# Kernel tuning notes

Hardware: AMD Instinct MI355X
Metric: run time of the kernel (lower is better)

## Reference

```python
import jax, jax.numpy as jnp
import numpy as np

EMBED_DIM = 1024
NUM_HEADS = 16
HEAD_DIM = EMBED_DIM // NUM_HEADS
LN_EPS = 1e-5


def setup_inputs() -> dict:
    key = jax.random.key(0)
    ks = jax.random.split(key, 12)
    B, SQ, SKV, E = 2, 1024, 4096, EMBED_DIM
    s = 1.0 / np.sqrt(E)
    return {
        "query": jax.random.normal(ks[0], (B, SQ, E), jnp.float32),
        "key_value": jax.random.normal(ks[1], (B, SKV, E), jnp.float32),
        "key_value_mask": jax.random.randint(ks[2], (B, SKV), 0, 2, jnp.int32),
        "Wq": jax.random.normal(ks[3], (E, E), jnp.float32) * s,
        "bq": jnp.zeros((E,), jnp.float32),
        "Wk": jax.random.normal(ks[4], (E, E), jnp.float32) * s,
        "bk": jnp.zeros((E,), jnp.float32),
        "Wv": jax.random.normal(ks[5], (E, E), jnp.float32) * s,
        "bv": jnp.zeros((E,), jnp.float32),
        "Wo": jax.random.normal(ks[6], (E, E), jnp.float32) * s,
        "bo": jnp.zeros((E,), jnp.float32),
        "ln_gamma": jnp.ones((E,), jnp.float32),
        "ln_beta": jnp.zeros((E,), jnp.float32),
    }


def reference(query, key_value, key_value_mask, Wq, bq, Wk, bk, Wv, bv, Wo, bo, ln_gamma, ln_beta):
    B, SQ, E = query.shape
    SKV = key_value.shape[1]
    H, D = NUM_HEADS, HEAD_DIM
    # projections (dropout is eval-mode identity)
    q = (query @ Wq.T + bq).reshape(B, SQ, H, D).transpose(0, 2, 1, 3)      # b h sq d
    k = (key_value @ Wk.T + bk).reshape(B, SKV, H, D).transpose(0, 2, 1, 3)  # b h skv d
    v = (key_value @ Wv.T + bv).reshape(B, SKV, H, D).transpose(0, 2, 1, 3)
    scale = jnp.sqrt(jnp.asarray(D, q.dtype))
    scores = jnp.einsum('bhqd,bhkd->bhqk', q, k) / scale                     # b h sq skv
    mask = (key_value_mask != 0)[:, None, None, :]                           # b 1 1 skv
    scores = jnp.where(mask, scores, jnp.asarray(-jnp.inf, scores.dtype))
    attn = jax.nn.softmax(scores, axis=-1)
    out = jnp.einsum('bhqk,bhkd->bhqd', attn, v)
    out = out.transpose(0, 2, 1, 3).reshape(B, SQ, E)
    out = out @ Wo.T + bo
    # post-LN residual
    x = query + out
    mu = jnp.mean(x, axis=-1, keepdims=True)
    var = jnp.mean(jnp.square(x - mu), axis=-1, keepdims=True)
    return (x - mu) * jax.lax.rsqrt(var + LN_EPS) * ln_gamma + ln_beta
```

## Files before the change

### kernel.cpp

```cpp
#include <hip/hip_runtime.h>
#include <cstdint>


typedef __bf16 bf16x8_t  __attribute__((ext_vector_type(8)));
typedef float  f32x4_t   __attribute__((ext_vector_type(4)));
typedef float  f32x16_t  __attribute__((ext_vector_type(16)));

#define E_DIM 1024
#define NH    16
#define HD    64
#define SCALE_L2E 0.1803368804f

__device__ __forceinline__ unsigned short f32_bf16(float f) {
    union { float f; unsigned int u; } v; v.f = f;
    unsigned int u = v.u;
    unsigned int r = (u + 0x7fffu + ((u >> 16) & 1u)) >> 16;
    return (unsigned short)r;
}

__device__ __forceinline__ unsigned pack_bf16(float a, float b) {
    __bf16 x = (__bf16)a, y = (__bf16)b;
    unsigned short ux = __builtin_bit_cast(unsigned short, x);
    unsigned short uy = __builtin_bit_cast(unsigned short, y);
    return (unsigned)ux | ((unsigned)uy << 16);
}

__device__ __forceinline__ void gld16(const unsigned short* g, unsigned short* l) {
    __builtin_amdgcn_global_load_lds(
        (const __attribute__((address_space(1))) unsigned int*)g,
        (__attribute__((address_space(3))) unsigned int*)l, 16, 0, 0);
}

__device__ __forceinline__ bf16x8_t ld16g(const unsigned short* p) {
    union { uint4 u; bf16x8_t f; } v;
    v.u = *reinterpret_cast<const uint4*>(p);
    return v.f;
}

__global__ void cast_all(const float* __restrict__ q, const float* __restrict__ kv,
                         const float* __restrict__ wq, const float* __restrict__ wk,
                         const float* __restrict__ wv, const float* __restrict__ wo,
                         unsigned short* __restrict__ Xq, unsigned short* __restrict__ Xkv,
                         unsigned short* __restrict__ Wqb, unsigned short* __restrict__ Wkb,
                         unsigned short* __restrict__ Wvb, unsigned short* __restrict__ Wob,
                         const int* __restrict__ msk, float* __restrict__ Sub) {
    __shared__ int red[4];
    if (blockIdx.x >= 14336) {
        int b = blockIdx.x - 14336, t = threadIdx.x;
        int s = 0;
#pragma unroll
        for (int k = 0; k < 16; k++) s += (msk[b * 4096 + k * 256 + t] != 0);
#pragma unroll
        for (int off = 32; off >= 1; off >>= 1) s += __shfl_xor(s, off, 64);
        if ((t & 63) == 0) red[t >> 6] = s;
        __syncthreads();
        if (t == 0)
            Sub[b] = (float)(4096 - (red[0] + red[1] + red[2] + red[3]));
        return;
    }
    long i = (long)blockIdx.x * 256 + threadIdx.x;
    const float* src; unsigned short* dst; long off;
    if (i < 2621440) {
        if (i < 524288) { src = q;  dst = Xq;  off = i; }
        else            { src = kv; dst = Xkv; off = i - 524288; }
    } else {
        long j = i - 2621440;
        int w = (int)(j >> 18); off = j & 262143;
        src = (w == 0) ? wq : (w == 1) ? wk : (w == 2) ? wv : wo;
        dst = (w == 0) ? Wqb : (w == 1) ? Wkb : (w == 2) ? Wvb : Wob;
    }
    float4 v = reinterpret_cast<const float4*>(src)[off];
    ushort4 o;
    o.x = f32_bf16(v.x); o.y = f32_bf16(v.y);
    o.z = f32_bf16(v.z); o.w = f32_bf16(v.w);
    reinterpret_cast<ushort4*>(dst)[off] = o;
}

#define BK 64

__global__ __launch_bounds__(256) void gemm_qkv(
    const unsigned short* __restrict__ Xq,
    const unsigned short* __restrict__ Xkv,
    const unsigned short* __restrict__ Wqb,
    const unsigned short* __restrict__ Wkb,
    const unsigned short* __restrict__ Wvb,
    const float* __restrict__ bq,
    const float* __restrict__ bk,
    const float* __restrict__ bv,
    unsigned short* __restrict__ Qout,
    unsigned short* __restrict__ Kout,
    unsigned short* __restrict__ Vout,
    const int* __restrict__ kvm)
{
    __shared__ __align__(16) unsigned short As[128 * BK];
    __shared__ __align__(16) unsigned short Bs[128 * BK];
    int bid  = blockIdx.x;
    int tid  = threadIdx.x;
    int lane = tid & 63;
    int wvu  = __builtin_amdgcn_readfirstlane(tid >> 6);
    int l15  = lane & 15, quad = lane >> 4, x7 = l15 & 7;

    if (bid < 1024) {
        int xcd  = bid & 7;
        int j    = bid >> 3;
        int mt   = xcd * 8 + (j >> 4);
        int sel  = j & 15;
        int isV  = sel >= 8;
        int m0   = mt * 128;
        int n0   = (sel & 7) * 128;
        const unsigned short* W = isV ? Wvb : Wkb;
        const float* bias = isV ? bv : bk;
        int wm   = ((tid >> 6) >> 1) * 64, wn = ((tid >> 6) & 1) * 64;

        f32x4_t acc[4][4];
#pragma unroll
        for (int i = 0; i < 4; i++)
#pragma unroll
            for (int jj = 0; jj < 4; jj++) acc[i][jj] = (f32x4_t)(0.f);

        for (int k0 = 0; k0 < 1024; k0 += BK) {
            __syncthreads();
#pragma unroll
            for (int i = 0; i < 4; i++) {
                int s = (i * 4 + wvu) * 64 + lane;
                int row = s >> 3, pcol = ((s & 7) ^ (row & 7)) << 3;
                gld16(&Xkv[(long)(m0 + row) * 1024 + k0 + pcol], &As[(i * 4 + wvu) * 512]);
                gld16(&W[(long)(n0 + row) * 1024 + k0 + pcol], &Bs[(i * 4 + wvu) * 512]);
            }
            __syncthreads();
            const char* Ab = (const char*)As;
            const char* Bb = (const char*)Bs;
#pragma unroll
            for (int ks = 0; ks < 2; ks++) {
                int pos = (((ks << 2) + quad) ^ x7) << 4;
                bf16x8_t af[4], bf[4];
#pragma unroll
                for (int mi = 0; mi < 4; mi++)
                    af[mi] = *reinterpret_cast<const bf16x8_t*>(
                        Ab + (wm + mi * 16 + l15) * 128 + pos);
#pragma unroll
                for (int ni = 0; ni < 4; ni++)
                    bf[ni] = *reinterpret_cast<const bf16x8_t*>(
                        Bb + (wn + ni * 16 + l15) * 128 + pos);
#pragma unroll
                for (int mi = 0; mi < 4; mi++)
#pragma unroll
                    for (int ni = 0; ni < 4; ni++)
                        acc[mi][ni] = __builtin_amdgcn_mfma_f32_16x16x32_bf16(
                            af[mi], bf[ni], acc[mi][ni], 0, 0, 0);
            }
        }
        int4 mk[4];
#pragma unroll
        for (int mi = 0; mi < 4; mi++) {
            int mg0 = m0 + wm + mi * 16 + quad * 4;
            mk[mi] = *reinterpret_cast<const int4*>(&kvm[mg0]);
        }
        if (!isV) {
#pragma unroll
            for (int mi = 0; mi < 4; mi++)
#pragma unroll
                for (int ni = 0; ni < 4; ni++) {
                    int n = n0 + wn + ni * 16 + l15;
                    float bvv = bias[n];
                    int h = n >> 6, d = n & 63;
#pragma unroll
                    for (int r = 0; r < 4; r++) {
                        int mg = m0 + wm + mi * 16 + quad * 4 + r;
                        int b = mg >> 12, s = mg & 4095;
                        unsigned short val = (&mk[mi].x)[r]
                            ? f32_bf16(acc[mi][ni][r] + bvv) : (unsigned short)0;
                        Kout[(((b * NH + h) << 12) + s) * HD + d] = val;
                    }
                }
        } else {
#pragma unroll
            for (int mi = 0; mi < 4; mi++)
#pragma unroll
                for (int ni = 0; ni < 4; ni++) {
                    int n = n0 + wn + ni * 16 + l15;
                    float bvv = bias[n];
                    int h = n >> 6, d = n & 63;
                    int mg0 = m0 + wm + mi * 16 + quad * 4;
                    int b = mg0 >> 12, s = mg0 & 4095;
                    ushort4 w;
                    w.x = mk[mi].x ? f32_bf16(acc[mi][ni][0] + bvv) : (unsigned short)0;
                    w.y = mk[mi].y ? f32_bf16(acc[mi][ni][1] + bvv) : (unsigned short)0;
                    w.z = mk[mi].z ? f32_bf16(acc[mi][ni][2] + bvv) : (unsigned short)0;
                    w.w = mk[mi].w ? f32_bf16(acc[mi][ni][3] + bvv) : (unsigned short)0;
                    *reinterpret_cast<ushort4*>(
                        &Vout[(((b * NH + h) * HD + d) << 12) + s]) = w;
                }
        }
    } else {
        int t    = bid - 1024;
        int xcd  = bid & 7;
        int j    = t >> 3;
        int mt   = xcd * 4 + (j >> 3);
        int m0   = mt * 64;
        int n0   = (j & 7) * 128;
        int wm   = ((tid >> 6) >> 1) * 32, wn = ((tid >> 6) & 1) * 64;

        f32x4_t acc[2][4];
#pragma unroll
        for (int i = 0; i < 2; i++)
#pragma unroll
            for (int jj = 0; jj < 4; jj++) acc[i][jj] = (f32x4_t)(0.f);

        for (int k0 = 0; k0 < 1024; k0 += BK) {
            __syncthreads();
#pragma unroll
            for (int i = 0; i < 2; i++) {
                int s = (i * 4 + wvu) * 64 + lane;
                int row = s >> 3, pcol = ((s & 7) ^ (row & 7)) << 3;
                gld16(&Xq[(long)(m0 + row) * 1024 + k0 + pcol], &As[(i * 4 + wvu) * 512]);
            }
#pragma unroll
            for (int i = 0; i < 4; i++) {
                int s = (i * 4 + wvu) * 64 + lane;
                int row = s >> 3, pcol = ((s & 7) ^ (row & 7)) << 3;
                gld16(&Wqb[(long)(n0 + row) * 1024 + k0 + pcol], &Bs[(i * 4 + wvu) * 512]);
            }
            __syncthreads();
            const char* Ab = (const char*)As;
            const char* Bb = (const char*)Bs;
#pragma unroll
            for (int ks = 0; ks < 2; ks++) {
                int pos = (((ks << 2) + quad) ^ x7) << 4;
                bf16x8_t af[2], bf[4];
#pragma unroll
                for (int mi = 0; mi < 2; mi++)
                    af[mi] = *reinterpret_cast<const bf16x8_t*>(
                        Ab + (wm + mi * 16 + l15) * 128 + pos);
#pragma unroll
                for (int ni = 0; ni < 4; ni++)
                    bf[ni] = *reinterpret_cast<const bf16x8_t*>(
                        Bb + (wn + ni * 16 + l15) * 128 + pos);
#pragma unroll
                for (int mi = 0; mi < 2; mi++)
#pragma unroll
                    for (int ni = 0; ni < 4; ni++)
                        acc[mi][ni] = __builtin_amdgcn_mfma_f32_16x16x32_bf16(
                            af[mi], bf[ni], acc[mi][ni], 0, 0, 0);
            }
        }
#pragma unroll
        for (int mi = 0; mi < 2; mi++)
#pragma unroll
            for (int ni = 0; ni < 4; ni++) {
                int n = n0 + wn + ni * 16 + l15;
                float bvq = bq[n];
                int h = n >> 6, d = n & 63;
#pragma unroll
                for (int r = 0; r < 4; r++) {
                    int mg = m0 + wm + mi * 16 + quad * 4 + r;
                    int b = mg >> 10, s = mg & 1023;
                    Qout[(((b * NH + h) << 10) + s) * HD + d] =
                        f32_bf16((acc[mi][ni][r] + bvq) * SCALE_L2E);
                }
            }
    }
}

__global__ __launch_bounds__(256) void gemm_oproj(
    const unsigned short* __restrict__ A,
    const unsigned short* __restrict__ W,
    const float* __restrict__ bias,
    const float* __restrict__ resid,
    float* __restrict__ xout)
{
    __shared__ __align__(16) unsigned short As[32 * BK];
    __shared__ __align__(16) unsigned short Bs[64 * BK];
    int tid  = threadIdx.x;
    int m0   = blockIdx.y * 32;
    int n0   = blockIdx.x * 64;
    int lane = tid & 63;
    int wvu  = __builtin_amdgcn_readfirstlane(tid >> 6);
    int l15  = lane & 15, quad = lane >> 4, x7 = l15 & 7;
    int wn   = (tid >> 6) * 16;

    f32x4_t acc[2];
    acc[0] = (f32x4_t)(0.f); acc[1] = (f32x4_t)(0.f);

    for (int k0 = 0; k0 < 1024; k0 += BK) {
        __syncthreads();
        {
            int s = wvu * 64 + lane;
            int row = s >> 3, pcol = ((s & 7) ^ (row & 7)) << 3;
            gld16(&A[(long)(m0 + row) * 1024 + k0 + pcol], &As[wvu * 512]);
        }
#pragma unroll
        for (int i = 0; i < 2; i++) {
            int s = (i * 4 + wvu) * 64 + lane;
            int row = s >> 3, pcol = ((s & 7) ^ (row & 7)) << 3;
            gld16(&W[(long)(n0 + row) * 1024 + k0 + pcol], &Bs[(i * 4 + wvu) * 512]);
        }
        __syncthreads();
        const char* Ab = (const char*)As;
        const char* Bb = (const char*)Bs;
#pragma unroll
        for (int ks = 0; ks < 2; ks++) {
            int pos = (((ks << 2) + quad) ^ x7) << 4;
            bf16x8_t af[2], bf;
#pragma unroll
            for (int mi = 0; mi < 2; mi++)
                af[mi] = *reinterpret_cast<const bf16x8_t*>(
                    Ab + (mi * 16 + l15) * 128 + pos);
            bf = *reinterpret_cast<const bf16x8_t*>(
                Bb + (wn + l15) * 128 + pos);
#pragma unroll
            for (int mi = 0; mi < 2; mi++)
                acc[mi] = __builtin_amdgcn_mfma_f32_16x16x32_bf16(
                    af[mi], bf, acc[mi], 0, 0, 0);
        }
    }
    int n = n0 + wn + l15;
    float bv = bias[n];
#pragma unroll
    for (int mi = 0; mi < 2; mi++)
#pragma unroll
        for (int r = 0; r < 4; r++) {
            int mg = m0 + mi * 16 + quad * 4 + r;
            xout[mg * 1024 + n] = acc[mi][r] + bv + resid[mg * 1024 + n];
        }
}

__global__ __launch_bounds__(512, 4) void attn_kernel(
    const unsigned short* __restrict__ Q,
    const unsigned short* __restrict__ K,
    const unsigned short* __restrict__ VT,
    float* __restrict__ Osc,
    float* __restrict__ Lsc)
{
    __shared__ __align__(16) union {
        struct { unsigned short Kb[2][8192]; unsigned short Vb[2][8192]; } st;
        struct { float OL[4][2048]; float ls[128]; } mg;
    } sm;

    int tid  = threadIdx.x;
    int lane = tid & 63;
    int w    = tid >> 6;
    int wvu  = __builtin_amdgcn_readfirstlane(w);
    int l31  = lane & 31, hw = lane >> 5;
    int qsub = w & 3, kvsub = w >> 2;

    int bid  = blockIdx.x;
    int xcd  = bid & 7, gidx = bid >> 3;
    int bh   = xcd * 4 + (gidx & 3);
    int rest = gidx >> 2;
    int q0   = (rest & 7) * 128;
    int bhalf = rest >> 3;

    const unsigned short* Kg = K + ((long)bh * 4096 + bhalf * 2048) * HD;
    const unsigned short* Vg = VT + (long)bh * HD * 4096 + bhalf * 2048;
    const unsigned short* Qb = Q + ((long)bh * 1024 + q0) * HD;

    bf16x8_t qfr[4];
#pragma unroll
    for (int ks = 0; ks < 4; ks++)
        qfr[ks] = ld16g(Qb + (qsub * 32 + l31) * HD + ks * 16 + hw * 8);

    f32x16_t oacc[2];
    oacc[0] = (f32x16_t)(0.f); oacc[1] = (f32x16_t)(0.f);
    float l_run = 0.f;

    auto stage = [&](int kt, int bufi) {
#pragma unroll
        for (int i = 0; i < 2; i++) {
            int s = (i * 8 + wvu) * 64 + lane;
            int krow = s >> 3, kpc = ((s & 7) ^ (krow & 7)) << 3;
            gld16(&Kg[(long)(kt * 128 + krow) * HD + kpc],
                  &sm.st.Kb[bufi][(i * 8 + wvu) * 512]);
            int vrow = s >> 4, vpc = ((s & 15) ^ (vrow & 15)) << 3;
            gld16(&Vg[(long)vrow * 4096 + kt * 128 + vpc],
                  &sm.st.Vb[bufi][(i * 8 + wvu) * 512]);
        }
    };

    const char* Kc = (const char*)sm.st.Kb;
    const char* Vc = (const char*)sm.st.Vb;

    stage(0, 0);
#pragma unroll 2
    for (int kt = 0; kt < 16; kt++) {
        __syncthreads();
        if (kt + 1 < 16) stage(kt + 1, (kt + 1) & 1);
        int bo = (kt & 1) * 16384;

#pragma unroll
        for (int t = 0; t < 2; t++) {
            f32x16_t sa = (f32x16_t)(0.f);
            int krow = kvsub * 64 + t * 32 + l31;
            __builtin_amdgcn_s_setprio(1);
#pragma unroll
            for (int ks = 0; ks < 4; ks++) {
                int phys = (ks * 2 + hw) ^ (krow & 7);
                bf16x8_t kf = *reinterpret_cast<const bf16x8_t*>(
                    Kc + bo + krow * 128 + phys * 16);
                sa = __builtin_amdgcn_mfma_f32_32x32x16_bf16(kf, qfr[ks], sa, 0, 0, 0);
            }
            __builtin_amdgcn_s_setprio(0);

            float pv[16];
#pragma unroll
            for (int r = 0; r < 16; r++) {
                float e;
                asm("v_exp_f32 %0, %1" : "=v"(e) : "v"(sa[r]));
                pv[r] = e;
            }
            float s0 = (pv[0] + pv[1]) + (pv[2] + pv[3]);
            float s1 = (pv[4] + pv[5]) + (pv[6] + pv[7]);
            float s2 = (pv[8] + pv[9]) + (pv[10] + pv[11]);
            float s3 = (pv[12] + pv[13]) + (pv[14] + pv[15]);
            l_run += (s0 + s1) + (s2 + s3);
            unsigned pku[8];
#pragma unroll
            for (int s4 = 0; s4 < 4; s4++) {
                pku[s4 * 2 + 0] = pack_bf16(pv[s4 * 4 + 0], pv[s4 * 4 + 1]);
                pku[s4 * 2 + 1] = pack_bf16(pv[s4 * 4 + 2], pv[s4 * 4 + 3]);
            }

            __builtin_amdgcn_s_setprio(1);
#pragma unroll
            for (int ks2 = 0; ks2 < 2; ks2++) {
                unsigned x0 = pku[(ks2 * 2) * 2 + 0];
                unsigned x1 = pku[(ks2 * 2) * 2 + 1];
                unsigned z0 = pku[(ks2 * 2 + 1) * 2 + 0];
                unsigned z1 = pku[(ks2 * 2 + 1) * 2 + 1];
                asm("v_permlane32_swap_b32 %0, %1" : "+v"(x0), "+v"(z0));
                asm("v_permlane32_swap_b32 %0, %1" : "+v"(x1), "+v"(z1));
                union { uint4 u; bf16x8_t f; } bw;
                bw.u.x = x0; bw.u.y = x1; bw.u.z = z0; bw.u.w = z1;
                int c = kvsub * 8 + t * 4 + ks2 * 2 + hw;
#pragma unroll
                for (int ds = 0; ds < 2; ds++) {
                    int vrow = ds * 32 + l31;
                    int phys = c ^ (vrow & 15);
                    bf16x8_t va = *reinterpret_cast<const bf16x8_t*>(
                        Vc + bo + vrow * 256 + phys * 16);
                    oacc[ds] = __builtin_amdgcn_mfma_f32_32x32x16_bf16(
                        va, bw.f, oacc[ds], 0, 0, 0);
                }
            }
            __builtin_amdgcn_s_setprio(0);
        }
    }

    l_run += __shfl_xor(l_run, 32, 64);
    __syncthreads();
    if (kvsub == 1) {
        float* OL = sm.mg.OL[qsub];
#pragma unroll
        for (int ds = 0; ds < 2; ds++)
#pragma unroll
            for (int r = 0; r < 16; r++) {
                int d = ds * 32 + (r & 3) + 8 * (r >> 2) + 4 * hw;
                OL[d * 32 + l31] = oacc[ds][r];
            }
        if (hw == 0) sm.mg.ls[qsub * 32 + l31] = l_run;
    }
    __syncthreads();
    if (kvsub == 0) {
        const float* OL = sm.mg.OL[qsub];
        int q = q0 + qsub * 32 + l31;
        long obase = (((long)bhalf * 32 + bh) * 64) * 1024;
#pragma unroll
        for (int ds = 0; ds < 2; ds++)
#pragma unroll
            for (int r = 0; r < 16; r++) {
                int d = ds * 32 + (r & 3) + 8 * (r >> 2) + 4 * hw;
                Osc[obase + (long)d * 1024 + q] = oacc[ds][r] + OL[d * 32 + l31];
            }
        if (hw == 0)
            Lsc[((long)bhalf * 32 + bh) * 1024 + q] = l_run + sm.mg.ls[qsub * 32 + l31];
    }
}

__global__ __launch_bounds__(256) void attn_merge(
    const float* __restrict__ Osc, const float* __restrict__ Lsc,
    const float* __restrict__ Sub, unsigned short* __restrict__ AO)
{
    __shared__ unsigned short T[64 * 66];
    int t = threadIdx.x, w = t >> 6, lane = t & 63;
    int bh = blockIdx.y, b = bh >> 4, h = bh & 15;
    int q0 = blockIdx.x * 64;
    int q = q0 + lane;

    float ls = Lsc[(long)bh * 1024 + q]
             + Lsc[(long)(32 + bh) * 1024 + q] - Sub[b];
    float inv = __builtin_amdgcn_rcpf(ls);
    inv = inv * (2.f - ls * inv);

#pragma unroll
    for (int dd = 0; dd < 16; dd++) {
        int d = w * 16 + dd;
        long base = (long)bh * 64 * 1024 + (long)d * 1024 + q;
        float o = Osc[base] + Osc[base + 32l * 64 * 1024];
        T[lane * 66 + d] = f32_bf16(o * inv);
    }
    __syncthreads();
    int q2 = t >> 2, c16 = (t & 3) * 16;
    unsigned ov[8];
#pragma unroll
    for (int j = 0; j < 8; j++)
        ov[j] = *reinterpret_cast<const unsigned*>(&T[q2 * 66 + c16 + j * 2]);
    unsigned short* dst = &AO[((long)(b * 1024 + q0 + q2)) * E_DIM + h * HD + c16];
    reinterpret_cast<uint4*>(dst)[0] = make_uint4(ov[0], ov[1], ov[2], ov[3]);
    reinterpret_cast<uint4*>(dst)[1] = make_uint4(ov[4], ov[5], ov[6], ov[7]);
}

__global__ __launch_bounds__(256) void ln_kernel(
    const float* __restrict__ x, const float* __restrict__ g,
    const float* __restrict__ be, float* __restrict__ out)
{
    __shared__ float red[8];
    int row = blockIdx.x, tid = threadIdx.x;
    float4 v = reinterpret_cast<const float4*>(x)[row * 256 + tid];
    float s  = v.x + v.y + v.z + v.w;
    float sq = v.x * v.x + v.y * v.y + v.z * v.z + v.w * v.w;
#pragma unroll
    for (int off = 32; off >= 1; off >>= 1) {
        s  += __shfl_xor(s,  off, 64);
        sq += __shfl_xor(sq, off, 64);
    }
    if ((tid & 63) == 0) { red[tid >> 6] = s; red[4 + (tid >> 6)] = sq; }
    __syncthreads();
    s  = red[0] + red[1] + red[2] + red[3];
    sq = red[4] + red[5] + red[6] + red[7];
    float mu  = s * (1.f / 1024.f);
    float var = sq * (1.f / 1024.f) - mu * mu;
    float rs  = rsqrtf(var + 1e-5f);
    int c = tid * 4;
    float4 o;
    o.x = (v.x - mu) * rs * g[c]     + be[c];
    o.y = (v.y - mu) * rs * g[c + 1] + be[c + 1];
    o.z = (v.z - mu) * rs * g[c + 2] + be[c + 2];
    o.w = (v.w - mu) * rs * g[c + 3] + be[c + 3];
    reinterpret_cast<float4*>(out)[row * 256 + tid] = o;
}

extern "C" void kernel_launch(void* const* d_in, const int* in_sizes, int n_in,
                              void* d_out, int out_size, void* d_ws, size_t ws_size,
                              hipStream_t stream) {
    const float* query     = (const float*)d_in[0];
    const float* key_value = (const float*)d_in[1];
    const int*   kv_mask   = (const int*)d_in[2];
    const float* Wq = (const float*)d_in[3];
    const float* bq = (const float*)d_in[4];
    const float* Wk = (const float*)d_in[5];
    const float* bk = (const float*)d_in[6];
    const float* Wv = (const float*)d_in[7];
    const float* bv = (const float*)d_in[8];
    const float* Wo = (const float*)d_in[9];
    const float* bo = (const float*)d_in[10];
    const float* ln_g = (const float*)d_in[11];
    const float* ln_b = (const float*)d_in[12];
    float* out = (float*)d_out;

    char* ws = (char*)d_ws;
    unsigned short* Xq  = (unsigned short*)(ws);
    unsigned short* Xkv = (unsigned short*)(ws + (4ll  << 20));
    unsigned short* Wqb = (unsigned short*)(ws + (20ll << 20));
    unsigned short* Wkb = (unsigned short*)(ws + (22ll << 20));
    unsigned short* Wvb = (unsigned short*)(ws + (24ll << 20));
    float*          Osc = (float*)(ws);
    unsigned short* Kh  = (unsigned short*)(ws + (32ll << 20));
    unsigned short* VTh = (unsigned short*)(ws + (48ll << 20));
    unsigned short* AO  = (unsigned short*)(ws + (64ll << 20));
    float*          Xr  = (float*)(ws + (68ll << 20));
    float*          Lsc = (float*)(ws + (76ll << 20));
    float*          Sub = (float*)(ws + (77ll << 20));
    unsigned short* Qh  = (unsigned short*)(ws + (80ll << 20));
    unsigned short* Wob = (unsigned short*)(ws + (84ll << 20));

    cast_all<<<14338, 256, 0, stream>>>(query, key_value, Wq, Wk, Wv, Wo,
                                        Xq, Xkv, Wqb, Wkb, Wvb, Wob,
                                        kv_mask, Sub);

    gemm_qkv<<<1280, 256, 0, stream>>>(Xq, Xkv, Wqb, Wkb, Wvb, bq, bk, bv,
                                       Qh, Kh, VTh, kv_mask);

    attn_kernel<<<512, 512, 0, stream>>>(Qh, Kh, VTh, Osc, Lsc);
    attn_merge<<<dim3(16, 32), 256, 0, stream>>>(Osc, Lsc, Sub, AO);

    gemm_oproj<<<dim3(16, 64), 256, 0, stream>>>(AO, Wob, bo, query, Xr);

    ln_kernel<<<2048, 256, 0, stream>>>(Xr, ln_g, ln_b, out);
}
```

Measured before the change: 234.9 us.

## Fuse attention split-KV merge into attention kernel by splitting KV across waves

Each block now covers 64 queries over the full 4096-key range instead of 128 queries over half the keys. The KV split moves inside the block across four wave groups, which are reduced through shared memory. The normalized bf16 output is written to AO directly, so the fp32 partial-output and row-sum buffers and the separate merge kernel go away. The costs are a 4-way shared-memory reduction instead of a 2-way one, and each block now streams twice as many K/V tiles for half as many queries, which doubles total K/V traffic.

```diff
diff --git a/kernel.cpp b/kernel.cpp
--- a/kernel.cpp
+++ b/kernel.cpp
@@ -329,12 +329,12 @@
     const unsigned short* __restrict__ Q,
     const unsigned short* __restrict__ K,
     const unsigned short* __restrict__ VT,
-    float* __restrict__ Osc,
-    float* __restrict__ Lsc)
+    const float* __restrict__ Sub,
+    unsigned short* __restrict__ AO)
 {
     __shared__ __align__(16) union {
         struct { unsigned short Kb[2][8192]; unsigned short Vb[2][8192]; } st;
-        struct { float OL[4][2048]; float ls[128]; } mg;
+        struct { float OL[6][2048]; float ls[256]; unsigned short T[64 * 66]; } mg;
     } sm;
 
     int tid  = threadIdx.x;
@@ -342,17 +342,16 @@
     int w    = tid >> 6;
     int wvu  = __builtin_amdgcn_readfirstlane(w);
     int l31  = lane & 31, hw = lane >> 5;
-    int qsub = w & 3, kvsub = w >> 2;
+    int qsub = w & 1, kvsub = w >> 1;
 
     int bid  = blockIdx.x;
     int xcd  = bid & 7, gidx = bid >> 3;
     int bh   = xcd * 4 + (gidx & 3);
-    int rest = gidx >> 2;
-    int q0   = (rest & 7) * 128;
-    int bhalf = rest >> 3;
-
-    const unsigned short* Kg = K + ((long)bh * 4096 + bhalf * 2048) * HD;
-    const unsigned short* Vg = VT + (long)bh * HD * 4096 + bhalf * 2048;
+    int q0   = (gidx >> 2) * 64;
+    int b    = bh >> 4, h = bh & 15;
+
+    const unsigned short* Kg = K + (long)bh * 4096 * HD;
+    const unsigned short* Vg = VT + (long)bh * HD * 4096;
     const unsigned short* Qb = Q + ((long)bh * 1024 + q0) * HD;
 
     bf16x8_t qfr[4];
@@ -382,74 +381,71 @@
 
     stage(0, 0);
 #pragma unroll 2
-    for (int kt = 0; kt < 16; kt++) {
+    for (int kt = 0; kt < 32; kt++) {
         __syncthreads();
-        if (kt + 1 < 16) stage(kt + 1, (kt + 1) & 1);
+        if (kt + 1 < 32) stage(kt + 1, (kt + 1) & 1);
         int bo = (kt & 1) * 16384;
 
-#pragma unroll
-        for (int t = 0; t < 2; t++) {
-            f32x16_t sa = (f32x16_t)(0.f);
-            int krow = kvsub * 64 + t * 32 + l31;
-            __builtin_amdgcn_s_setprio(1);
-#pragma unroll
-            for (int ks = 0; ks < 4; ks++) {
-                int phys = (ks * 2 + hw) ^ (krow & 7);
-                bf16x8_t kf = *reinterpret_cast<const bf16x8_t*>(
-                    Kc + bo + krow * 128 + phys * 16);
-                sa = __builtin_amdgcn_mfma_f32_32x32x16_bf16(kf, qfr[ks], sa, 0, 0, 0);
-            }
-            __builtin_amdgcn_s_setprio(0);
-
-            float pv[16];
-#pragma unroll
-            for (int r = 0; r < 16; r++) {
-                float e;
-                asm("v_exp_f32 %0, %1" : "=v"(e) : "v"(sa[r]));
-                pv[r] = e;
-            }
-            float s0 = (pv[0] + pv[1]) + (pv[2] + pv[3]);
-            float s1 = (pv[4] + pv[5]) + (pv[6] + pv[7]);
-            float s2 = (pv[8] + pv[9]) + (pv[10] + pv[11]);
-            float s3 = (pv[12] + pv[13]) + (pv[14] + pv[15]);
-            l_run += (s0 + s1) + (s2 + s3);
-            unsigned pku[8];
-#pragma unroll
-            for (int s4 = 0; s4 < 4; s4++) {
-                pku[s4 * 2 + 0] = pack_bf16(pv[s4 * 4 + 0], pv[s4 * 4 + 1]);
-                pku[s4 * 2 + 1] = pack_bf16(pv[s4 * 4 + 2], pv[s4 * 4 + 3]);
-            }
-
-            __builtin_amdgcn_s_setprio(1);
-#pragma unroll
-            for (int ks2 = 0; ks2 < 2; ks2++) {
-                unsigned x0 = pku[(ks2 * 2) * 2 + 0];
-                unsigned x1 = pku[(ks2 * 2) * 2 + 1];
-                unsigned z0 = pku[(ks2 * 2 + 1) * 2 + 0];
-                unsigned z1 = pku[(ks2 * 2 + 1) * 2 + 1];
-                asm("v_permlane32_swap_b32 %0, %1" : "+v"(x0), "+v"(z0));
-                asm("v_permlane32_swap_b32 %0, %1" : "+v"(x1), "+v"(z1));
-                union { uint4 u; bf16x8_t f; } bw;
-                bw.u.x = x0; bw.u.y = x1; bw.u.z = z0; bw.u.w = z1;
-                int c = kvsub * 8 + t * 4 + ks2 * 2 + hw;
-#pragma unroll
-                for (int ds = 0; ds < 2; ds++) {
-                    int vrow = ds * 32 + l31;
-                    int phys = c ^ (vrow & 15);
-                    bf16x8_t va = *reinterpret_cast<const bf16x8_t*>(
-                        Vc + bo + vrow * 256 + phys * 16);
-                    oacc[ds] = __builtin_amdgcn_mfma_f32_32x32x16_bf16(
-                        va, bw.f, oacc[ds], 0, 0, 0);
-                }
-            }
-            __builtin_amdgcn_s_setprio(0);
-        }
+        f32x16_t sa = (f32x16_t)(0.f);
+        int krow = kvsub * 32 + l31;
+        __builtin_amdgcn_s_setprio(1);
+#pragma unroll
+        for (int ks = 0; ks < 4; ks++) {
+            int phys = (ks * 2 + hw) ^ (krow & 7);
+            bf16x8_t kf = *reinterpret_cast<const bf16x8_t*>(
+                Kc + bo + krow * 128 + phys * 16);
+            sa = __builtin_amdgcn_mfma_f32_32x32x16_bf16(kf, qfr[ks], sa, 0, 0, 0);
+        }
+        __builtin_amdgcn_s_setprio(0);
+
+        float pv[16];
+#pragma unroll
+        for (int r = 0; r < 16; r++) {
+            float e;
+            asm("v_exp_f32 %0, %1" : "=v"(e) : "v"(sa[r]));
+            pv[r] = e;
+        }
+        float s0 = (pv[0] + pv[1]) + (pv[2] + pv[3]);
+        float s1 = (pv[4] + pv[5]) + (pv[6] + pv[7]);
+        float s2 = (pv[8] + pv[9]) + (pv[10] + pv[11]);
+        float s3 = (pv[12] + pv[13]) + (pv[14] + pv[15]);
+        l_run += (s0 + s1) + (s2 + s3);
+        unsigned pku[8];
+#pragma unroll
+        for (int s4 = 0; s4 < 4; s4++) {
+            pku[s4 * 2 + 0] = pack_bf16(pv[s4 * 4 + 0], pv[s4 * 4 + 1]);
+            pku[s4 * 2 + 1] = pack_bf16(pv[s4 * 4 + 2], pv[s4 * 4 + 3]);
+        }
+
+        __builtin_amdgcn_s_setprio(1);
+#pragma unroll
+        for (int ks2 = 0; ks2 < 2; ks2++) {
+            unsigned x0 = pku[(ks2 * 2) * 2 + 0];
+            unsigned x1 = pku[(ks2 * 2) * 2 + 1];
+            unsigned z0 = pku[(ks2 * 2 + 1) * 2 + 0];
+            unsigned z1 = pku[(ks2 * 2 + 1) * 2 + 1];
+            asm("v_permlane32_swap_b32 %0, %1" : "+v"(x0), "+v"(z0));
+            asm("v_permlane32_swap_b32 %0, %1" : "+v"(x1), "+v"(z1));
+            union { uint4 u; bf16x8_t f; } bw;
+            bw.u.x = x0; bw.u.y = x1; bw.u.z = z0; bw.u.w = z1;
+            int c = kvsub * 4 + ks2 * 2 + hw;
+#pragma unroll
+            for (int ds = 0; ds < 2; ds++) {
+                int vrow = ds * 32 + l31;
+                int phys = c ^ (vrow & 15);
+                bf16x8_t va = *reinterpret_cast<const bf16x8_t*>(
+                    Vc + bo + vrow * 256 + phys * 16);
+                oacc[ds] = __builtin_amdgcn_mfma_f32_32x32x16_bf16(
+                    va, bw.f, oacc[ds], 0, 0, 0);
+            }
+        }
+        __builtin_amdgcn_s_setprio(0);
     }
 
     l_run += __shfl_xor(l_run, 32, 64);
     __syncthreads();
-    if (kvsub == 1) {
-        float* OL = sm.mg.OL[qsub];
+    if (kvsub != 0) {
+        float* OL = sm.mg.OL[(kvsub - 1) * 2 + qsub];
 #pragma unroll
         for (int ds = 0; ds < 2; ds++)
 #pragma unroll
@@ -457,56 +453,40 @@
                 int d = ds * 32 + (r & 3) + 8 * (r >> 2) + 4 * hw;
                 OL[d * 32 + l31] = oacc[ds][r];
             }
-        if (hw == 0) sm.mg.ls[qsub * 32 + l31] = l_run;
+        if (hw == 0) sm.mg.ls[(kvsub * 2 + qsub) * 32 + l31] = l_run;
     }
     __syncthreads();
     if (kvsub == 0) {
-        const float* OL = sm.mg.OL[qsub];
-        int q = q0 + qsub * 32 + l31;
-        long obase = (((long)bhalf * 32 + bh) * 64) * 1024;
+        float lt = l_run;
+#pragma unroll
+        for (int k = 1; k < 4; k++)
+            lt += sm.mg.ls[(k * 2 + qsub) * 32 + l31];
+        lt -= Sub[b];
+        float inv = __builtin_amdgcn_rcpf(lt);
+        inv = inv * (2.f - lt * inv);
+        int q = qsub * 32 + l31;
 #pragma unroll
         for (int ds = 0; ds < 2; ds++)
 #pragma unroll
             for (int r = 0; r < 16; r++) {
                 int d = ds * 32 + (r & 3) + 8 * (r >> 2) + 4 * hw;
-                Osc[obase + (long)d * 1024 + q] = oacc[ds][r] + OL[d * 32 + l31];
-            }
-        if (hw == 0)
-            Lsc[((long)bhalf * 32 + bh) * 1024 + q] = l_run + sm.mg.ls[qsub * 32 + l31];
-    }
-}
-
-__global__ __launch_bounds__(256) void attn_merge(
-    const float* __restrict__ Osc, const float* __restrict__ Lsc,
-    const float* __restrict__ Sub, unsigned short* __restrict__ AO)
-{
-    __shared__ unsigned short T[64 * 66];
-    int t = threadIdx.x, w = t >> 6, lane = t & 63;
-    int bh = blockIdx.y, b = bh >> 4, h = bh & 15;
-    int q0 = blockIdx.x * 64;
-    int q = q0 + lane;
-
-    float ls = Lsc[(long)bh * 1024 + q]
-             + Lsc[(long)(32 + bh) * 1024 + q] - Sub[b];
-    float inv = __builtin_amdgcn_rcpf(ls);
-    inv = inv * (2.f - ls * inv);
-
-#pragma unroll
-    for (int dd = 0; dd < 16; dd++) {
-        int d = w * 16 + dd;
-        long base = (long)bh * 64 * 1024 + (long)d * 1024 + q;
-        float o = Osc[base] + Osc[base + 32l * 64 * 1024];
-        T[lane * 66 + d] = f32_bf16(o * inv);
+                float o = oacc[ds][r];
+#pragma unroll
+                for (int k = 0; k < 3; k++)
+                    o += sm.mg.OL[k * 2 + qsub][d * 32 + l31];
+                sm.mg.T[q * 66 + d] = f32_bf16(o * inv);
+            }
     }
     __syncthreads();
-    int q2 = t >> 2, c16 = (t & 3) * 16;
-    unsigned ov[8];
-#pragma unroll
-    for (int j = 0; j < 8; j++)
-        ov[j] = *reinterpret_cast<const unsigned*>(&T[q2 * 66 + c16 + j * 2]);
-    unsigned short* dst = &AO[((long)(b * 1024 + q0 + q2)) * E_DIM + h * HD + c16];
-    reinterpret_cast<uint4*>(dst)[0] = make_uint4(ov[0], ov[1], ov[2], ov[3]);
-    reinterpret_cast<uint4*>(dst)[1] = make_uint4(ov[4], ov[5], ov[6], ov[7]);
+    {
+        int q2 = tid >> 3, c16 = (tid & 7) * 8;
+        unsigned ov[4];
+#pragma unroll
+        for (int j = 0; j < 4; j++)
+            ov[j] = *reinterpret_cast<const unsigned*>(&sm.mg.T[q2 * 66 + c16 + j * 2]);
+        unsigned short* dst = &AO[((long)(b * 1024 + q0 + q2)) * E_DIM + h * HD + c16];
+        reinterpret_cast<uint4*>(dst)[0] = make_uint4(ov[0], ov[1], ov[2], ov[3]);
+    }
 }
 
 __global__ __launch_bounds__(256) void ln_kernel(
@@ -563,12 +543,10 @@
     unsigned short* Wqb = (unsigned short*)(ws + (20ll << 20));
     unsigned short* Wkb = (unsigned short*)(ws + (22ll << 20));
     unsigned short* Wvb = (unsigned short*)(ws + (24ll << 20));
-    float*          Osc = (float*)(ws);
     unsigned short* Kh  = (unsigned short*)(ws + (32ll << 20));
     unsigned short* VTh = (unsigned short*)(ws + (48ll << 20));
     unsigned short* AO  = (unsigned short*)(ws + (64ll << 20));
     float*          Xr  = (float*)(ws + (68ll << 20));
-    float*          Lsc = (float*)(ws + (76ll << 20));
     float*          Sub = (float*)(ws + (77ll << 20));
     unsigned short* Qh  = (unsigned short*)(ws + (80ll << 20));
     unsigned short* Wob = (unsigned short*)(ws + (84ll << 20));
@@ -580,8 +558,7 @@
     gemm_qkv<<<1280, 256, 0, stream>>>(Xq, Xkv, Wqb, Wkb, Wvb, bq, bk, bv,
                                        Qh, Kh, VTh, kv_mask);
 
-    attn_kernel<<<512, 512, 0, stream>>>(Qh, Kh, VTh, Osc, Lsc);
-    attn_merge<<<dim3(16, 32), 256, 0, stream>>>(Osc, Lsc, Sub, AO);
+    attn_kernel<<<512, 512, 0, stream>>>(Qh, Kh, VTh, Sub, AO);
 
     gemm_oproj<<<dim3(16, 64), 256, 0, stream>>>(AO, Wob, bo, query, Xr);
 
```

Measured after the change: 229.6 us (median of 3 runs). -2.3%, faster.
